# Optimization experiments

Hardware: AMD Instinct MI355X
Metric: run time of the kernel (lower is better)

The kernel has to match this reference:

```python
import jax, jax.numpy as jnp
import numpy as np

K = 3   # num nearest neighbors (init k)
P = 2   # IDW power (init p)


def setup_inputs() -> dict:
    key = jax.random.key(0)
    k1, k2, k3, k4 = jax.random.split(key, 4)
    B, N, M, C = 8, 16384, 1024, 256
    xyz = jax.random.normal(k1, (B, N, 3), dtype=jnp.float32)
    sampled_xyz = jax.random.normal(k2, (B, M, 3), dtype=jnp.float32)
    sampled_features = jax.random.normal(k3, (B, M, C), dtype=jnp.float32)
    masks = jax.random.randint(k4, (B, N), 0, 2, dtype=jnp.int32)
    return {"xyz": xyz, "sampled_xyz": sampled_xyz,
            "sampled_features": sampled_features, "masks": masks}


def reference(xyz, sampled_xyz, sampled_features, masks):
    # xyz: [B,N,3], sampled_xyz: [B,M,3], sampled_features: [B,M,C], masks: [B,N]
    # Squared pairwise distances [B,N,M] (same math as the chunked torch loop).
    delta = xyz[:, :, None, :] - sampled_xyz[:, None, :, :]
    dists = jnp.sum(delta * delta, axis=-1)
    # k smallest distances -> negate and take top-k.
    neg_top, idx = jax.lax.top_k(-dists, K)          # [B,N,K]
    min_dists = jnp.maximum(-neg_top, 1e-10)
    weights = 1.0 / (min_dists ** P + 1e-10)
    weights = weights / jnp.sum(weights, axis=-1, keepdims=True)
    # Gather neighbor features: [B,N,K,C]
    gathered = jax.vmap(lambda f, i: f[i])(sampled_features, idx)
    interpolated = jnp.sum(gathered * weights[..., None], axis=2)  # [B,N,C]
    # Invalid (masked-out) rows stay zero, matching the padded scatter.
    valid = (masks != 0).astype(interpolated.dtype)
    return interpolated * valid[..., None]
```

## Files before the change

kernel.cpp:

```cpp
#include <hip/hip_runtime.h>

constexpr int B = 8;
constexpr int N = 16384;
constexpr int M = 1024;
constexpr int C = 256;
constexpr int PTS = 64;
constexpr int QW  = 4;

__global__ __launch_bounds__(256, 8) void upsample_idw_kernel(
    const float* __restrict__ xyz,
    const float* __restrict__ sxyz,
    const float* __restrict__ feats,
    const int*   __restrict__ masks,
    float*       __restrict__ out)
{
    const int tid = threadIdx.x;
    const int w   = tid >> 6;
    const int l   = tid & 63;
    const int blk = blockIdx.x;
    const int b     = blk >> 8;
    const int nbase = (blk & 255) << 6;

    __shared__ float4 s_cand[M];
    unsigned long long (*s_key)[QW][3] = (unsigned long long (*)[QW][3])s_cand;
    __shared__ float s_w[PTS][3];
    __shared__ int   s_j[PTS][4];

    {
        const float4* src4 = (const float4*)(sxyz + (size_t)b * (M * 3));
        const float4 t0 = src4[3 * tid + 0];
        const float4 t1 = src4[3 * tid + 1];
        const float4 t2 = src4[3 * tid + 2];
        s_cand[4 * tid + 0] = make_float4(t0.x, t0.y, t0.z, 0.f);
        s_cand[4 * tid + 1] = make_float4(t0.w, t1.x, t1.y, 0.f);
        s_cand[4 * tid + 2] = make_float4(t1.z, t1.w, t2.x, 0.f);
        s_cand[4 * tid + 3] = make_float4(t2.y, t2.z, t2.w, 0.f);
    }

    const int n = nbase + l;
    const float* xp = xyz + ((size_t)b * N + n) * 3;
    const float x = xp[0], y = xp[1], z = xp[2];
    __syncthreads();

    const float4* cp = s_cand + w * 256;

    float d0 = __builtin_inff(), d1 = __builtin_inff(), d2 = __builtin_inff();
    int   i0 = 0, i1 = 0, i2 = 0;

    #pragma unroll 8
    for (int m = 0; m < 256; ++m) {
        const float4 c = cp[m];
        const float dx = __fsub_rn(x, c.x);
        const float dy = __fsub_rn(y, c.y);
        const float dz = __fsub_rn(z, c.z);
        const float d  = __fadd_rn(__fadd_rn(__fmul_rn(dx, dx), __fmul_rn(dy, dy)),
                                   __fmul_rn(dz, dz));
        const bool lt0 = d < d0, lt1 = d < d1, lt2 = d < d2;
        i2 = lt1 ? i1 : (lt2 ? m : i2);
        i1 = lt0 ? i0 : (lt1 ? m : i1);
        i0 = lt0 ? m  : i0;
        const float nd2 = __builtin_amdgcn_fmed3f(d1, d2, d);
        const float nd1 = __builtin_amdgcn_fmed3f(d0, d1, d);
        d2 = nd2;
        d1 = nd1;
        d0 = fminf(d0, d);
    }
    __syncthreads();

    const unsigned base = (unsigned)(w * 256);
    s_key[l][w][0] = ((unsigned long long)__float_as_uint(d0) << 32) | (base + (unsigned)i0);
    s_key[l][w][1] = ((unsigned long long)__float_as_uint(d1) << 32) | (base + (unsigned)i1);
    s_key[l][w][2] = ((unsigned long long)__float_as_uint(d2) << 32) | (base + (unsigned)i2);
    __syncthreads();

    if (tid < PTS) {
        unsigned long long k0 = ~0ULL, k1 = ~0ULL, k2 = ~0ULL;
        #pragma unroll
        for (int q = 0; q < QW; ++q) {
            #pragma unroll
            for (int s = 0; s < 3; ++s) {
                const unsigned long long k = s_key[tid][q][s];
                const bool lt0 = k < k0, lt1 = k < k1, lt2 = k < k2;
                k2 = lt1 ? k1 : (lt2 ? k : k2);
                k1 = lt0 ? k0 : (lt1 ? k : k1);
                k0 = lt0 ? k  : k0;
            }
        }
        const float e0 = __uint_as_float((unsigned)(k0 >> 32));
        const float e1 = __uint_as_float((unsigned)(k1 >> 32));
        const float e2 = __uint_as_float((unsigned)(k2 >> 32));
        const float m0 = fmaxf(e0, 1e-10f);
        const float m1 = fmaxf(e1, 1e-10f);
        const float m2 = fmaxf(e2, 1e-10f);
        float w0 = 1.0f / (m0 * m0 + 1e-10f);
        float w1 = 1.0f / (m1 * m1 + 1e-10f);
        float w2 = 1.0f / (m2 * m2 + 1e-10f);
        const int valid = masks[(size_t)b * N + nbase + tid];
        const float scale = valid ? (1.0f / (w0 + w1 + w2)) : 0.0f;
        s_w[tid][0] = w0 * scale;
        s_w[tid][1] = w1 * scale;
        s_w[tid][2] = w2 * scale;
        s_j[tid][0] = (int)(unsigned)k0;
        s_j[tid][1] = (int)(unsigned)k1;
        s_j[tid][2] = (int)(unsigned)k2;
        s_j[tid][3] = valid;
    }
    __syncthreads();

    const int pq = tid >> 6;
    const int cq = tid & 63;
    const float4* Fb4 = (const float4*)(feats + (size_t)b * (M * C));
    float4* op4 = (float4*)(out + (((size_t)b * N + nbase) * C));

    for (int p0 = 0; p0 < PTS; p0 += 4) {
        const int p = p0 + pq;
        const int vld = __builtin_amdgcn_readfirstlane(s_j[p][3]);
        float4 acc = make_float4(0.f, 0.f, 0.f, 0.f);
        if (vld) {
            const int j0 = __builtin_amdgcn_readfirstlane(s_j[p][0]);
            const int j1 = __builtin_amdgcn_readfirstlane(s_j[p][1]);
            const int j2 = __builtin_amdgcn_readfirstlane(s_j[p][2]);
            const float w0 = __uint_as_float(
                __builtin_amdgcn_readfirstlane((int)__float_as_uint(s_w[p][0])));
            const float w1 = __uint_as_float(
                __builtin_amdgcn_readfirstlane((int)__float_as_uint(s_w[p][1])));
            const float w2 = __uint_as_float(
                __builtin_amdgcn_readfirstlane((int)__float_as_uint(s_w[p][2])));
            const float4 f0 = Fb4[j0 * 64 + cq];
            const float4 f1 = Fb4[j1 * 64 + cq];
            const float4 f2 = Fb4[j2 * 64 + cq];
            acc.x = fmaf(w2, f2.x, fmaf(w1, f1.x, w0 * f0.x));
            acc.y = fmaf(w2, f2.y, fmaf(w1, f1.y, w0 * f0.y));
            acc.z = fmaf(w2, f2.z, fmaf(w1, f1.z, w0 * f0.z));
            acc.w = fmaf(w2, f2.w, fmaf(w1, f1.w, w0 * f0.w));
        }
        op4[p * 64 + cq] = acc;
    }
}

extern "C" void kernel_launch(void* const* d_in, const int* in_sizes, int n_in,
                              void* d_out, int out_size, void* d_ws, size_t ws_size,
                              hipStream_t stream) {
    const float* xyz   = (const float*)d_in[0];
    const float* sxyz  = (const float*)d_in[1];
    const float* feats = (const float*)d_in[2];
    const int*   masks = (const int*)d_in[3];
    float*       out   = (float*)d_out;

    dim3 grid(B * N / PTS);
    dim3 block(256);
    hipLaunchKernelGGL(upsample_idw_kernel, grid, block, 0, stream,
                       xyz, sxyz, feats, masks, out);
}
```

Measured before the change: 74.40 us.

## Process two query points per thread across eight waves of 512-thread blocks

Each block now handles 128 points with 512 threads. Each of the 8 waves scans 128 candidates, and every thread keeps top-3 state for two query points, so each candidate loaded from LDS is reused twice. This halves LDS reads per distance and doubles independent work per thread, which adds ILP. The cost is more registers, a larger 8-way merge done by 128 threads, and larger blocks that may reduce occupancy.

```diff
diff --git a/kernel.cpp b/kernel.cpp
--- a/kernel.cpp
+++ b/kernel.cpp
@@ -4,10 +4,11 @@
 constexpr int N = 16384;
 constexpr int M = 1024;
 constexpr int C = 256;
-constexpr int PTS = 64;
-constexpr int QW  = 4;
+constexpr int PTS = 128;
+constexpr int NW  = 8;
+constexpr int CPW = M / NW;
 
-__global__ __launch_bounds__(256, 8) void upsample_idw_kernel(
+__global__ __launch_bounds__(512, 8) void upsample_idw_kernel(
     const float* __restrict__ xyz,
     const float* __restrict__ sxyz,
     const float* __restrict__ feats,
@@ -18,65 +19,85 @@
     const int w   = tid >> 6;
     const int l   = tid & 63;
     const int blk = blockIdx.x;
-    const int b     = blk >> 8;
-    const int nbase = (blk & 255) << 6;
+    const int b     = blk >> 7;
+    const int nbase = (blk & 127) << 7;
 
-    __shared__ float4 s_cand[M];
-    unsigned long long (*s_key)[QW][3] = (unsigned long long (*)[QW][3])s_cand;
+    __shared__ unsigned long long s_key[PTS][NW][3];
+    float4* s_cand = (float4*)&s_key[0][0][0];
     __shared__ float s_w[PTS][3];
     __shared__ int   s_j[PTS][4];
 
     {
-        const float4* src4 = (const float4*)(sxyz + (size_t)b * (M * 3));
-        const float4 t0 = src4[3 * tid + 0];
-        const float4 t1 = src4[3 * tid + 1];
-        const float4 t2 = src4[3 * tid + 2];
-        s_cand[4 * tid + 0] = make_float4(t0.x, t0.y, t0.z, 0.f);
-        s_cand[4 * tid + 1] = make_float4(t0.w, t1.x, t1.y, 0.f);
-        s_cand[4 * tid + 2] = make_float4(t1.z, t1.w, t2.x, 0.f);
-        s_cand[4 * tid + 3] = make_float4(t2.y, t2.z, t2.w, 0.f);
+        const float* sp = sxyz + (size_t)b * (M * 3);
+        #pragma unroll
+        for (int t = tid; t < M; t += 512) {
+            const float cx = sp[3 * t + 0];
+            const float cy = sp[3 * t + 1];
+            const float cz = sp[3 * t + 2];
+            s_cand[t] = make_float4(cx, cy, cz, 0.f);
+        }
     }
 
-    const int n = nbase + l;
-    const float* xp = xyz + ((size_t)b * N + n) * 3;
-    const float x = xp[0], y = xp[1], z = xp[2];
+    const float* xpA = xyz + ((size_t)b * N + nbase + l) * 3;
+    const float* xpB = xyz + ((size_t)b * N + nbase + l + 64) * 3;
+    const float xA = xpA[0], yA = xpA[1], zA = xpA[2];
+    const float xB = xpB[0], yB = xpB[1], zB = xpB[2];
     __syncthreads();
 
-    const float4* cp = s_cand + w * 256;
+    const float4* cp = s_cand + w * CPW;
 
-    float d0 = __builtin_inff(), d1 = __builtin_inff(), d2 = __builtin_inff();
-    int   i0 = 0, i1 = 0, i2 = 0;
+    float a0 = __builtin_inff(), a1 = __builtin_inff(), a2 = __builtin_inff();
+    float b0 = __builtin_inff(), b1 = __builtin_inff(), b2 = __builtin_inff();
+    int   ia0 = 0, ia1 = 0, ia2 = 0;
+    int   ib0 = 0, ib1 = 0, ib2 = 0;
 
-    #pragma unroll 8
-    for (int m = 0; m < 256; ++m) {
+    #pragma unroll 2
+    for (int m = 0; m < CPW; ++m) {
         const float4 c = cp[m];
-        const float dx = __fsub_rn(x, c.x);
-        const float dy = __fsub_rn(y, c.y);
-        const float dz = __fsub_rn(z, c.z);
-        const float d  = __fadd_rn(__fadd_rn(__fmul_rn(dx, dx), __fmul_rn(dy, dy)),
-                                   __fmul_rn(dz, dz));
-        const bool lt0 = d < d0, lt1 = d < d1, lt2 = d < d2;
-        i2 = lt1 ? i1 : (lt2 ? m : i2);
-        i1 = lt0 ? i0 : (lt1 ? m : i1);
-        i0 = lt0 ? m  : i0;
-        const float nd2 = __builtin_amdgcn_fmed3f(d1, d2, d);
-        const float nd1 = __builtin_amdgcn_fmed3f(d0, d1, d);
-        d2 = nd2;
-        d1 = nd1;
-        d0 = fminf(d0, d);
+        {
+            const float dx = __fsub_rn(xA, c.x);
+            const float dy = __fsub_rn(yA, c.y);
+            const float dz = __fsub_rn(zA, c.z);
+            const float d  = __fadd_rn(__fadd_rn(__fmul_rn(dx, dx), __fmul_rn(dy, dy)),
+                                       __fmul_rn(dz, dz));
+            const bool lt0 = d < a0, lt1 = d < a1, lt2 = d < a2;
+            ia2 = lt1 ? ia1 : (lt2 ? m : ia2);
+            ia1 = lt0 ? ia0 : (lt1 ? m : ia1);
+            ia0 = lt0 ? m   : ia0;
+            const float nd2 = __builtin_amdgcn_fmed3f(a1, a2, d);
+            const float nd1 = __builtin_amdgcn_fmed3f(a0, a1, d);
+            a2 = nd2; a1 = nd1; a0 = fminf(a0, d);
+        }
+        {
+            const float dx = __fsub_rn(xB, c.x);
+            const float dy = __fsub_rn(yB, c.y);
+            const float dz = __fsub_rn(zB, c.z);
+            const float d  = __fadd_rn(__fadd_rn(__fmul_rn(dx, dx), __fmul_rn(dy, dy)),
+                                       __fmul_rn(dz, dz));
+            const bool lt0 = d < b0, lt1 = d < b1, lt2 = d < b2;
+            ib2 = lt1 ? ib1 : (lt2 ? m : ib2);
+            ib1 = lt0 ? ib0 : (lt1 ? m : ib1);
+            ib0 = lt0 ? m   : ib0;
+            const float nd2 = __builtin_amdgcn_fmed3f(b1, b2, d);
+            const float nd1 = __builtin_amdgcn_fmed3f(b0, b1, d);
+            b2 = nd2; b1 = nd1; b0 = fminf(b0, d);
+        }
     }
     __syncthreads();
 
-    const unsigned base = (unsigned)(w * 256);
-    s_key[l][w][0] = ((unsigned long long)__float_as_uint(d0) << 32) | (base + (unsigned)i0);
-    s_key[l][w][1] = ((unsigned long long)__float_as_uint(d1) << 32) | (base + (unsigned)i1);
-    s_key[l][w][2] = ((unsigned long long)__float_as_uint(d2) << 32) | (base + (unsigned)i2);
+    const unsigned base = (unsigned)(w * CPW);
+    s_key[l][w][0]      = ((unsigned long long)__float_as_uint(a0) << 32) | (base + (unsigned)ia0);
+    s_key[l][w][1]      = ((unsigned long long)__float_as_uint(a1) << 32) | (base + (unsigned)ia1);
+    s_key[l][w][2]      = ((unsigned long long)__float_as_uint(a2) << 32) | (base + (unsigned)ia2);
+    s_key[l + 64][w][0] = ((unsigned long long)__float_as_uint(b0) << 32) | (base + (unsigned)ib0);
+    s_key[l + 64][w][1] = ((unsigned long long)__float_as_uint(b1) << 32) | (base + (unsigned)ib1);
+    s_key[l + 64][w][2] = ((unsigned long long)__float_as_uint(b2) << 32) | (base + (unsigned)ib2);
     __syncthreads();
 
     if (tid < PTS) {
         unsigned long long k0 = ~0ULL, k1 = ~0ULL, k2 = ~0ULL;
         #pragma unroll
-        for (int q = 0; q < QW; ++q) {
+        for (int q = 0; q < NW; ++q) {
             #pragma unroll
             for (int s = 0; s < 3; ++s) {
                 const unsigned long long k = s_key[tid][q][s];
@@ -112,7 +133,7 @@
     const float4* Fb4 = (const float4*)(feats + (size_t)b * (M * C));
     float4* op4 = (float4*)(out + (((size_t)b * N + nbase) * C));
 
-    for (int p0 = 0; p0 < PTS; p0 += 4) {
+    for (int p0 = 0; p0 < PTS; p0 += 8) {
         const int p = p0 + pq;
         const int vld = __builtin_amdgcn_readfirstlane(s_j[p][3]);
         float4 acc = make_float4(0.f, 0.f, 0.f, 0.f);
@@ -148,7 +169,7 @@
     float*       out   = (float*)d_out;
 
     dim3 grid(B * N / PTS);
-    dim3 block(256);
+    dim3 block(512);
     hipLaunchKernelGGL(upsample_idw_kernel, grid, block, 0, stream,
                        xyz, sxyz, feats, masks, out);
 }
```

New measurement: 79.93 us. 1.07x slower.
